# Performance work log

Hardware: AMD Instinct MI355X
Metric: run time of the kernel (lower is better)

## Reference

```python
import jax, jax.numpy as jnp
import numpy as np

B, S, E = 32, 128, 128
NQ, NS = 100000, 512
QN, SN = 4, 10
S_MAX = 4
NEG = -1e30


def setup_inputs() -> dict:
    key = jax.random.key(0)
    ks = jax.random.split(key, 24)
    def nrm(k, shape, sc):
        return jax.random.normal(k, shape, jnp.float32) * sc
    inp = {}
    inp['question'] = jax.random.randint(ks[0], (B, S), 0, NQ, jnp.int32)
    inp['response'] = jax.random.randint(ks[1], (B, S), 0, 2, jnp.int32)
    inp['mask'] = jax.random.randint(ks[2], (B, S), 0, 2, jnp.int32)
    inp['q_neighbors'] = jax.random.randint(ks[3], (NQ, QN), 0, NS, jnp.int32)
    inp['s_neighbors'] = jax.random.randint(ks[4], (NS, SN), 0, NQ, jnp.int32)
    sidx = jax.random.randint(ks[5], (NQ, S_MAX), 0, NS, jnp.int32)
    inp['qs_table'] = jnp.zeros((NQ, NS), jnp.float32).at[jnp.arange(NQ)[:, None], sidx].set(1.0)
    inp['emb_q'] = nrm(ks[6], (NQ, E), 1.0)
    inp['emb_s'] = nrm(ks[7], (NS, E), 1.0)
    inp['emb_r'] = nrm(ks[8], (2, E), 1.0)
    s_in = 1.0 / np.sqrt(2 * E).astype(np.float32)
    s_e = 1.0 / np.sqrt(E).astype(np.float32)
    inp['W_ih'] = nrm(ks[9], (4 * E, 2 * E), s_in)
    inp['b_ih'] = nrm(ks[10], (4 * E,), s_in)
    inp['b_hh'] = nrm(ks[11], (4 * E,), s_in)
    inp['W_agg'] = nrm(ks[12], (3, E, E), s_e)
    inp['b_agg'] = nrm(ks[13], (3, E), s_e)
    inp['W_last'] = nrm(ks[14], (E, E), s_e)
    inp['b_last'] = nrm(ks[15], (E,), s_e)
    inp['W_query'] = nrm(ks[16], (E, E), s_e)
    inp['b_query'] = nrm(ks[17], (E,), s_e)
    inp['W_key'] = nrm(ks[18], (E, E), s_e)
    inp['b_key'] = nrm(ks[19], (E,), s_e)
    inp['w_W'] = nrm(ks[20], (2 * E,), s_in)
    inp['b_W'] = nrm(ks[21], (), s_in)
    return inp


def _forward(question, response, mask, q_neighbors, s_neighbors, qs_table,
             emb_q, emb_s, emb_r, W_ih, b_ih, b_hh, W_agg, b_agg, W_last, b_last,
             W_query, b_query, W_key, b_key, w_W, b_W):
    Bq, Sq = question.shape
    Ed = emb_q.shape[1]
    AGG = W_agg.shape[0]
    w_q, w_k = w_W[:Ed], w_W[Ed:]
    c_pad = jnp.tanh(b_query) @ w_k  # attention logit piece of an all-zero padded state
    pos = jnp.arange(Sq)

    def step(state_history, xs):
        t, q_t, r_t, m_t, q_next = xs
        # ---- multi-hop neighbor gather (q -> s -> q -> s) ----
        n1 = q_neighbors[q_t]              # [B,QN] skill ids
        n2 = s_neighbors[n1]               # [B,QN,SN] question ids
        n3 = q_neighbors[n2]               # [B,QN,SN,QN] skill ids
        e = [emb_q[q_t], emb_s[n1], emb_q[n2], emb_s[n3]]
        # triangular mean-aggregate (dropout is identity in eval mode)
        for i in range(AGG):
            for j in range(AGG - i):
                e[j] = jnp.tanh((e[j + 1].mean(-2) + e[j]) @ W_agg[j].T + b_agg[j])
        agg = jnp.tanh(e[0] @ W_last.T + b_last)
        emb_qt = jnp.where((m_t == 1)[:, None], agg, emb_q[q_t])
        # ---- LSTMCell with zero initial (h, c): W_hh @ 0 drops out, b_hh remains ----
        x = jnp.concatenate([emb_qt, emb_r[r_t]], -1)
        gates = x @ W_ih.T + b_ih + b_hh
        gi, gf, gg, go = jnp.split(gates, 4, -1)
        h = jax.nn.sigmoid(go) * jnp.tanh(jax.nn.sigmoid(gi) * jnp.tanh(gg))
        # ---- skills related to next question; zero-padded rows contribute exactly 0 ----
        vals, sidx = jax.lax.top_k(qs_table[q_next], S_MAX)
        emb_sk = emb_s[sidx] * (vals > 0.0)[..., None]
        qs_concat = jnp.concatenate([emb_q[q_next][:, None], emb_sk], 1)  # [B,1+S_MAX,E]
        # ---- hard recap: history steps whose question is a 2-hop neighbor of q_next ----
        q_rel = s_neighbors[q_neighbors[q_next]].reshape(Bq, -1)          # [B,QN*SN]
        matches = (question[:, :, None] == q_rel[:, None, :]).any(-1) & (pos[None, :] < t)
        n_sel = matches.sum(-1)
        P = (jnp.max(n_sel) - n_sel).astype(jnp.float32)  # zero-pad count to per-batch max
        # ---- predict: MLP_W(concat(Q,K)) is rank-1 => logit = a[b,q] + c[b,s] ----
        a = jnp.tanh(qs_concat @ W_key.T + b_key) @ w_q + b_W             # [B,Qd]
        c_hist = jnp.tanh(state_history @ W_query.T + b_query) @ w_k      # [B,S]
        c_cur = jnp.tanh(h @ W_query.T + b_query) @ w_k                   # [B]
        lh = jnp.where(matches[:, None, :], a[:, :, None] + c_hist[:, None, :], NEG)
        lc = a + c_cur[:, None]
        lp = a + c_pad
        m = jnp.maximum(jnp.maximum(lh.max(-1), lc), lp)
        Eh = jnp.exp(lh - m[:, :, None])
        Ec = jnp.exp(lc - m)
        Ep = jnp.exp(lp - m)
        g_hist = jnp.einsum('bqe,bse->bqs', qs_concat, state_history)
        g_cur = jnp.einsum('bqe,be->bq', qs_concat, h)
        denom = Eh.sum(-1) + Ec + P[:, None] * Ep  # zero-pad states counted analytically
        num = (Eh * g_hist).sum(-1) + Ec * g_cur   # pads multiply g=0 -> no numerator term
        y = jax.nn.sigmoid(jnp.sum(num / denom, axis=1))
        # original skips the state write at t == 0 (slot 0 stays zero forever)
        state_history = state_history.at[:, t].set(jnp.where(t > 0, h, jnp.zeros_like(h)))
        return state_history, y

    ts = jnp.arange(Sq - 1)
    xs = (ts, question[:, :-1].T, response[:, :-1].T, mask[:, :-1].T, question[:, 1:].T)
    init = jnp.zeros((Bq, Sq, Ed), jnp.float32)
    _, ys = jax.lax.scan(step, init, xs)
    return jnp.zeros((Bq, Sq), jnp.float32).at[:, 0].set(0.5).at[:, 1:].set(ys.T)


def reference(question, response, mask, q_neighbors, s_neighbors, qs_table,
              emb_q, emb_s, emb_r, W_ih, b_ih, b_hh, W_agg, b_agg, W_last, b_last,
              W_query, b_query, W_key, b_key, w_W, b_W):
    return _forward(question, response, mask, q_neighbors, s_neighbors, qs_table,
                    emb_q, emb_s, emb_r, W_ih, b_ih, b_hh, W_agg, b_agg, W_last, b_last,
                    W_query, b_query, W_key, b_key, w_W, b_W)
```

## Files before the change

kernel.cpp:

```cpp
#include <hip/hip_runtime.h>
#include <stdint.h>

#define NB 32
#define SEQ 128
#define EMB 128
#define NSTEP 127
#define NS 512

__device__ __forceinline__ float ftanh(float x){ float e=__expf(2.f*x); return 1.f-2.f/(e+1.f); }
__device__ __forceinline__ float fsig(float x){ return 1.f/(1.f+__expf(-x)); }
__device__ __forceinline__ float4 ld4(const float* p){ return *(const float4*)p; }

#define FMA_COL(acc, xv) \
  acc.x = fmaf(xv.x, w0.x, fmaf(xv.y, w1.x, fmaf(xv.z, w2.x, fmaf(xv.w, w3.x, acc.x)))); \
  acc.y = fmaf(xv.x, w0.y, fmaf(xv.y, w1.y, fmaf(xv.z, w2.y, fmaf(xv.w, w3.y, acc.y)))); \
  acc.z = fmaf(xv.x, w0.z, fmaf(xv.y, w1.z, fmaf(xv.z, w2.z, fmaf(xv.w, w3.z, acc.z)))); \
  acc.w = fmaf(xv.x, w0.w, fmaf(xv.y, w1.w, fmaf(xv.z, w2.w, fmaf(xv.w, w3.w, acc.w))));

template<int K, int XS>
__device__ __forceinline__ void gemm8(const float* __restrict__ WT, int NEtot,
                                      const float* __restrict__ Xl,
                                      const float* __restrict__ bias,
                                      float* __restrict__ outb )
{
  const int tid = threadIdx.x;
  const int et = tid & 31;
  const int rt = tid >> 5;
  const float* wp = WT + et*4;
  const float* xr = Xl + rt*XS;
  constexpr int G = K/4;
  float4 acc = {0.f,0.f,0.f,0.f};
  float4 w0 = ld4(wp);
  float4 w1 = ld4(wp + NEtot);
  float4 w2 = ld4(wp + 2*NEtot);
  float4 w3 = ld4(wp + 3*NEtot);
  float4 xa = ld4(xr);
  #pragma unroll 4
  for (int g = 0; g < G-1; ++g) {
    const float* wn = wp + (size_t)(4*(g+1))*NEtot;
    float4 m0 = ld4(wn);
    float4 m1 = ld4(wn + NEtot);
    float4 m2 = ld4(wn + 2*NEtot);
    float4 m3 = ld4(wn + 3*NEtot);
    float4 xb = ld4(xr + 4*(g+1));
    FMA_COL(acc, xa);
    w0=m0; w1=m1; w2=m2; w3=m3; xa=xb;
  }
  FMA_COL(acc, xa);
  float4 bb = ld4(bias + et*4);
  acc.x+=bb.x; acc.y+=bb.y; acc.z+=bb.z; acc.w+=bb.w;
  *(float4*)(outb + rt*132 + et*4) = acc;
}
#undef FMA_COL

__global__ __launch_bounds__(256) void k_T(
    const float* __restrict__ W_agg, const float* __restrict__ W_last,
    const float* __restrict__ W_query, const float* __restrict__ W_ih,
    const float* __restrict__ b_ih, const float* __restrict__ b_hh,
    const float* __restrict__ b_query, const float* __restrict__ w_W,
    float* __restrict__ WT012, float* __restrict__ WLT, float* __restrict__ WQT,
    float* __restrict__ WIHT, float* __restrict__ BIH, float* __restrict__ CPAD,
    float* __restrict__ G1, int* __restrict__ Pmaxi)
{
  const int gid = blockIdx.x*256 + threadIdx.x;
  const int gsz = gridDim.x*256;
  for (int i = gid; i < 49152; i += gsz) {
    int j = i >> 14, rem = i & 16383, k = rem >> 7, e = rem & 127;
    WT012[i] = W_agg[j*16384 + e*128 + k];
  }
  for (int i = gid; i < 16384; i += gsz) {
    int k = i >> 7, e = i & 127;
    WLT[i] = W_last[e*128 + k];
    WQT[i] = W_query[e*128 + k];
  }
  for (int i = gid; i < 131072; i += gsz) {
    int k = i >> 9, e = i & 511;
    WIHT[i] = W_ih[e*256 + k];
  }
  for (int i = gid; i < 65536; i += gsz) G1[i] = 0.f;
  for (int i = gid; i < 512; i += gsz) BIH[i] = b_ih[i] + b_hh[i];
  for (int i = gid; i < 128; i += gsz) Pmaxi[i] = 0;
  if (blockIdx.x == 0) {
    __shared__ float red[256];
    float v = (threadIdx.x < 128) ? ftanh(b_query[threadIdx.x]) * w_W[128 + threadIdx.x] : 0.f;
    red[threadIdx.x] = v; __syncthreads();
    #pragma unroll
    for (int s = 128; s > 0; s >>= 1) {
      if (threadIdx.x < s) red[threadIdx.x] += red[threadIdx.x + s];
      __syncthreads();
    }
    if (threadIdx.x == 0) CPAD[0] = red[0];
  }
}

__global__ __launch_bounds__(256) void k_pre(
    const int* __restrict__ s_neighbors, const int* __restrict__ q_neighbors,
    const float* __restrict__ emb_q, const float* __restrict__ emb_s,
    const float* __restrict__ WT012, const float* __restrict__ b_agg,
    float* __restrict__ E1, float* __restrict__ G1)
{
  __shared__ float XA[8*132];
  __shared__ float XB[8*132];
  __shared__ int idx[80];
  __shared__ int n3[32];
  const int tid = threadIdx.x;
  const int blk = blockIdx.x;
  if (blk < 64) {
    const int s0 = blk*8;
    if (tid < 80) idx[tid] = s_neighbors[s0*10 + tid];
    __syncthreads();
    {
      int r = tid >> 5, e4 = (tid & 31) << 2;
      float4 a = ld4(emb_s + (size_t)(s0+r)*128 + e4);
      float sx=0,sy=0,sz=0,sw=0;
      #pragma unroll
      for (int jj = 0; jj < 10; ++jj) {
        float4 q = ld4(emb_q + (size_t)idx[r*10+jj]*128 + e4);
        sx+=q.x; sy+=q.y; sz+=q.z; sw+=q.w;
      }
      float4 o; o.x=a.x+0.1f*sx; o.y=a.y+0.1f*sy; o.z=a.z+0.1f*sz; o.w=a.w+0.1f*sw;
      *(float4*)(XA + r*132 + e4) = o;
    }
    __syncthreads();
    gemm8<128,132>(WT012 + 16384, 128, XA, b_agg + 128, XB);
    __syncthreads();
    for (int f = tid; f < 1024; f += 256) {
      int r = f >> 7, e = f & 127;
      E1[(size_t)(s0+r)*128 + e] = ftanh(XB[r*132 + e]);
    }
  } else {
    const int p0 = (blk-64)*8;
    if (tid < 8) idx[tid] = s_neighbors[p0 + tid];
    __syncthreads();
    if (tid < 32) n3[tid] = q_neighbors[(size_t)idx[tid>>2]*4 + (tid&3)];
    __syncthreads();
    {
      int r = tid >> 5, e4 = (tid & 31) << 2;
      float4 a = ld4(emb_q + (size_t)idx[r]*128 + e4);
      float sx=0,sy=0,sz=0,sw=0;
      #pragma unroll
      for (int k = 0; k < 4; ++k) {
        float4 q = ld4(emb_s + (size_t)n3[r*4+k]*128 + e4);
        sx+=q.x; sy+=q.y; sz+=q.z; sw+=q.w;
      }
      float4 o; o.x=a.x+0.25f*sx; o.y=a.y+0.25f*sy; o.z=a.z+0.25f*sz; o.w=a.w+0.25f*sw;
      *(float4*)(XA + r*132 + e4) = o;
    }
    __syncthreads();
    gemm8<128,132>(WT012 + 32768, 128, XA, b_agg + 256, XB);
    __syncthreads();
    for (int f = tid; f < 1024; f += 256) {
      int r = f >> 7, e = f & 127;
      atomicAdd(&G1[(size_t)((p0+r)/10)*128 + e], ftanh(XB[r*132 + e]));
    }
  }
}

__global__ __launch_bounds__(256) void k_pre2(
    const float* __restrict__ E1, const float* __restrict__ G1,
    const float* __restrict__ WT012, const float* __restrict__ b_agg,
    float* __restrict__ E2)
{
  __shared__ float XA[8*132];
  __shared__ float XB[8*132];
  const int tid = threadIdx.x;
  const int s0 = blockIdx.x*8;
  for (int f = tid; f < 1024; f += 256) {
    int r = f >> 7, e = f & 127;
    XA[r*132 + e] = 0.1f*G1[(size_t)(s0+r)*128 + e] + E1[(size_t)(s0+r)*128 + e];
  }
  __syncthreads();
  gemm8<128,132>(WT012 + 16384, 128, XA, b_agg + 128, XB);
  __syncthreads();
  for (int f = tid; f < 1024; f += 256) {
    int r = f >> 7, e = f & 127;
    E2[(size_t)(s0+r)*128 + e] = ftanh(XB[r*132 + e]);
  }
}

__global__ __launch_bounds__(256) void k_chain(
    const int* __restrict__ question, const int* __restrict__ response,
    const int* __restrict__ maskp, const int* __restrict__ q_neighbors,
    const float* __restrict__ emb_q, const float* __restrict__ emb_s,
    const float* __restrict__ emb_r,
    const float* __restrict__ WT012, const float* __restrict__ WLT,
    const float* __restrict__ WQT, const float* __restrict__ WIHT,
    const float* __restrict__ BIH,
    const float* __restrict__ b_agg, const float* __restrict__ b_last,
    const float* __restrict__ b_query, const float* __restrict__ w_W,
    const float* __restrict__ E1, const float* __restrict__ E2,
    float* __restrict__ Hfull, float* __restrict__ Cq)
{
  __shared__ float XA[8*132];
  __shared__ float XB[8*132];
  __shared__ float M1[8*132];
  __shared__ float M2[8*132];
  __shared__ float XC[8*264];
  __shared__ int qts[8], rts[8], mts[8], n1s[32];

  const int tid = threadIdx.x;
  const int blk = blockIdx.x;

  if (tid < 8) {
    int rid = blk*8 + tid;
    int b = rid / 127, t = rid - b*127;
    qts[tid] = question[b*SEQ + t];
    rts[tid] = response[b*SEQ + t];
    mts[tid] = maskp[b*SEQ + t];
  }
  __syncthreads();
  if (tid < 32) n1s[tid] = q_neighbors[(size_t)qts[tid>>2]*4 + (tid&3)];
  __syncthreads();
  {
    int r = tid >> 5, e4 = (tid & 31) << 2;
    const int* nn = n1s + r*4;
    float4 a = ld4(emb_q + (size_t)qts[r]*128 + e4);
    float s1x=0,s1y=0,s1z=0,s1w=0, s2x=0,s2y=0,s2z=0,s2w=0, s3x=0,s3y=0,s3z=0,s3w=0;
    #pragma unroll
    for (int i = 0; i < 4; ++i) {
      float4 q1 = ld4(emb_s + (size_t)nn[i]*128 + e4);
      float4 q2 = ld4(E1 + (size_t)nn[i]*128 + e4);
      float4 q3 = ld4(E2 + (size_t)nn[i]*128 + e4);
      s1x+=q1.x; s1y+=q1.y; s1z+=q1.z; s1w+=q1.w;
      s2x+=q2.x; s2y+=q2.y; s2z+=q2.z; s2w+=q2.w;
      s3x+=q3.x; s3y+=q3.y; s3z+=q3.z; s3w+=q3.w;
    }
    float4 o; o.x=a.x+0.25f*s1x; o.y=a.y+0.25f*s1y; o.z=a.z+0.25f*s1z; o.w=a.w+0.25f*s1w;
    *(float4*)(XA + r*132 + e4) = o;
    float4 p; p.x=0.25f*s2x; p.y=0.25f*s2y; p.z=0.25f*s2z; p.w=0.25f*s2w;
    *(float4*)(M1 + r*132 + e4) = p;
    float4 u; u.x=0.25f*s3x; u.y=0.25f*s3y; u.z=0.25f*s3z; u.w=0.25f*s3w;
    *(float4*)(M2 + r*132 + e4) = u;
  }
  __syncthreads();
  gemm8<128,132>(WT012, 128, XA, b_agg, XB);
  __syncthreads();
  for (int f = tid; f < 1056; f += 256) XB[f] = M1[f] + ftanh(XB[f]);
  __syncthreads();
  gemm8<128,132>(WT012, 128, XB, b_agg, XA);
  __syncthreads();
  for (int f = tid; f < 1056; f += 256) XA[f] = M2[f] + ftanh(XA[f]);
  __syncthreads();
  gemm8<128,132>(WT012, 128, XA, b_agg, XB);
  __syncthreads();
  for (int f = tid; f < 1056; f += 256) XB[f] = ftanh(XB[f]);
  __syncthreads();
  gemm8<128,132>(WLT, 128, XB, b_last, XA);
  __syncthreads();
  for (int f = tid; f < 1024; f += 256) {
    int r = f >> 7, e = f & 127;
    float agg = ftanh(XA[r*132 + e]);
    XC[r*264 + e] = (mts[r] == 1) ? agg : emb_q[(size_t)qts[r]*128 + e];
    XC[r*264 + 128 + e] = emb_r[rts[r]*128 + e];
  }
  __syncthreads();
  gemm8<256,264>(WIHT,       512, XC, BIH,       XA);
  gemm8<256,264>(WIHT + 256, 512, XC, BIH + 256, XB);
  gemm8<256,264>(WIHT + 384, 512, XC, BIH + 384, M1);
  __syncthreads();
  for (int f = tid; f < 1024; f += 256) {
    int r = f >> 7, e = f & 127;
    float gi = XA[r*132 + e], gg = XB[r*132 + e], go = M1[r*132 + e];
    float h = fsig(go) * ftanh(fsig(gi) * ftanh(gg));
    XC[r*264 + e] = h;
    Hfull[(size_t)(blk*8 + r)*128 + e] = h;
  }
  __syncthreads();
  gemm8<128,264>(WQT, 128, XC, b_query, XA);
  __syncthreads();
  {
    const int et = tid & 31, rt = tid >> 5;
    float4 o = ld4(XA + rt*132 + et*4);
    float4 wv = ld4(w_W + 128 + et*4);
    float s = ftanh(o.x)*wv.x + ftanh(o.y)*wv.y + ftanh(o.z)*wv.z + ftanh(o.w)*wv.w;
    #pragma unroll
    for (int off = 16; off > 0; off >>= 1) s += __shfl_down(s, off);
    if (et == 0) Cq[blk*8 + rt] = s;
  }
}

__global__ __launch_bounds__(128) void k_match(
    const int* __restrict__ question, const int* __restrict__ q_neighbors,
    const int* __restrict__ s_neighbors,
    int* __restrict__ nsel, unsigned long long* __restrict__ mwords,
    int* __restrict__ Pmaxi)
{
  __shared__ int nq[4];
  __shared__ int qr[40];
  __shared__ unsigned long long wv[2];
  const int tid = threadIdx.x;
  const int t = blockIdx.x;
  for (int bb = 0; bb < 8; ++bb) {
    const int b = blockIdx.y*8 + bb;
    const int q_next = question[b*SEQ + t + 1];
    if (tid < 4) nq[tid] = q_neighbors[(size_t)q_next*4 + tid];
    __syncthreads();
    if (tid < 40) qr[tid] = s_neighbors[(size_t)nq[tid/10]*10 + tid%10];
    __syncthreads();
    bool pred = false;
    if (tid < t) {
      int qp = question[b*SEQ + tid];
      #pragma unroll 8
      for (int i = 0; i < 40; ++i) pred |= (qp == qr[i]);
    }
    unsigned long long bal = __ballot(pred);
    if ((tid & 63) == 0) wv[tid >> 6] = bal;
    __syncthreads();
    if (tid == 0) {
      mwords[((size_t)b*NSTEP + t)*2 + 0] = wv[0];
      mwords[((size_t)b*NSTEP + t)*2 + 1] = wv[1];
      int ns = __popcll(wv[0]) + __popcll(wv[1]);
      nsel[b*NSTEP + t] = ns;
      atomicMax(&Pmaxi[t], ns);
    }
    __syncthreads();
  }
}

__device__ __forceinline__ float wredsum(float v) {
  #pragma unroll
  for (int o = 32; o > 0; o >>= 1) v += __shfl_down(v, o);
  return v;
}
__device__ __forceinline__ float wredmax(float v) {
  #pragma unroll
  for (int o = 32; o > 0; o >>= 1) v = fmaxf(v, __shfl_down(v, o));
  return v;
}

__global__ __launch_bounds__(128) void k_attn(
    const int* __restrict__ question, const float* __restrict__ qs_table,
    const float* __restrict__ emb_q, const float* __restrict__ emb_s,
    const float* __restrict__ CPAD,
    const float* __restrict__ Hfull, const float* __restrict__ Cq,
    const int* __restrict__ nsel, const unsigned long long* __restrict__ mwords,
    const int* __restrict__ Pmaxi, float* __restrict__ out)
{
  __shared__ float us[128];
  __shared__ int cols[8];
  __shared__ int cnt;
  __shared__ float smx[2];
  __shared__ float s3[2][3];
  const int tid = threadIdx.x;
  const int wid = tid >> 6;
  const int bid = blockIdx.x;
  const int b = bid / NSTEP, t = bid % NSTEP;
  const size_t bt = (size_t)b*NSTEP + t;
  const int q_next = question[b*SEQ + t + 1];

  if (tid == 0) cnt = 0;
  __syncthreads();
  #pragma unroll
  for (int m = 0; m < 4; ++m) {
    int c = tid + 128*m;
    float v = qs_table[(size_t)q_next*NS + c];
    if (v > 0.f) {
      int p = atomicAdd(&cnt, 1);
      if (p < 8) cols[p] = c;
    }
  }
  __syncthreads();
  const int nc = min(cnt, 4);
  {
    float ue = emb_q[(size_t)q_next*EMB + tid];
    for (int i = 0; i < nc; ++i) ue += emb_s[(size_t)cols[i]*EMB + tid];
    us[tid] = ue;
  }
  const float c_pad = CPAD[0];
  const float P = (float)(Pmaxi[t] - nsel[bt]);

  const unsigned long long w0 = mwords[bt*2 + 0];
  const unsigned long long w1 = mwords[bt*2 + 1];
  const bool matched = (tid < 64) ? ((w0 >> tid) & 1ull)
                                  : ((w1 >> (tid - 64)) & 1ull);
  const float c_cur = Cq[bt];
  float Cp = matched ? ((tid == 0) ? c_pad : Cq[(size_t)b*NSTEP + tid]) : -3.0e38f;
  float mh = wredmax(Cp);
  if ((tid & 63) == 0) smx[wid] = mh;
  __syncthreads();
  float M = fmaxf(fmaxf(smx[0], smx[1]), fmaxf(c_cur, c_pad));
  float wgt = matched ? __expf(Cp - M) : 0.f;
  float dotp = 0.f;
  if (matched && tid >= 1) {
    const float* hp = Hfull + ((size_t)b*NSTEP + tid)*EMB;
    float s = 0.f;
    #pragma unroll 8
    for (int e = 0; e < 128; e += 4) {
      float4 h4 = ld4(hp + e);
      s = fmaf(us[e],h4.x, fmaf(us[e+1],h4.y, fmaf(us[e+2],h4.z, fmaf(us[e+3],h4.w, s))));
    }
    dotp = s;
  }
  float gcp = us[tid] * Hfull[bt*EMB + tid];
  float a0 = wredsum(wgt);
  float a1 = wredsum(wgt * dotp);
  float a2 = wredsum(gcp);
  if ((tid & 63) == 0) { s3[wid][0] = a0; s3[wid][1] = a1; s3[wid][2] = a2; }
  __syncthreads();
  if (tid == 0) {
    float Sexp = s3[0][0] + s3[1][0];
    float Snum = s3[0][1] + s3[1][1];
    float gc   = s3[0][2] + s3[1][2];
    float Ec = __expf(c_cur - M), Ep = __expf(c_pad - M);
    float D = Sexp + Ec + P * Ep;
    float numt = Snum + Ec * gc;
    out[b*SEQ + t + 1] = fsig(numt / D);
    if (t == 0) out[b*SEQ] = 0.5f;
  }
}

extern "C" void kernel_launch(void* const* d_in, const int* in_sizes, int n_in,
                              void* d_out, int out_size, void* d_ws, size_t ws_size,
                              hipStream_t stream) {
  const int* question    = (const int*)d_in[0];
  const int* response    = (const int*)d_in[1];
  const int* maskp       = (const int*)d_in[2];
  const int* q_neighbors = (const int*)d_in[3];
  const int* s_neighbors = (const int*)d_in[4];
  const float* qs_table  = (const float*)d_in[5];
  const float* emb_q     = (const float*)d_in[6];
  const float* emb_s     = (const float*)d_in[7];
  const float* emb_r     = (const float*)d_in[8];
  const float* W_ih      = (const float*)d_in[9];
  const float* b_ih      = (const float*)d_in[10];
  const float* b_hh      = (const float*)d_in[11];
  const float* W_agg     = (const float*)d_in[12];
  const float* b_agg     = (const float*)d_in[13];
  const float* W_last    = (const float*)d_in[14];
  const float* b_last    = (const float*)d_in[15];
  const float* W_query   = (const float*)d_in[16];
  const float* b_query   = (const float*)d_in[17];
  const float* w_W       = (const float*)d_in[20];
  float* out = (float*)d_out;

  float* ws = (float*)d_ws;
  float* WT012 = ws;
  float* WLT   = ws + 49152;
  float* WQT   = ws + 65536;
  float* WIHT  = ws + 81920;
  float* BIH   = ws + 212992;
  float* CPAD  = ws + 213504;
  float* E1    = ws + 213520;
  float* G1    = ws + 279056;
  float* E2    = ws + 344592;
  float* Hfull = ws + 410128;
  float* Cq    = ws + 930320;
  int*   Pmaxi = (int*)(ws + 934384);
  int*   nselp = (int*)(ws + 934512);
  unsigned long long* mwords =
      (unsigned long long*)(((uintptr_t)(ws + 938576) + 15) & ~(uintptr_t)15);

  k_T<<<dim3(64), dim3(256), 0, stream>>>(
      W_agg, W_last, W_query, W_ih, b_ih, b_hh, b_query, w_W,
      WT012, WLT, WQT, WIHT, BIH, CPAD, G1, Pmaxi);
  k_pre<<<dim3(704), dim3(256), 0, stream>>>(
      s_neighbors, q_neighbors, emb_q, emb_s, WT012, b_agg, E1, G1);
  k_pre2<<<dim3(64), dim3(256), 0, stream>>>(E1, G1, WT012, b_agg, E2);
  k_chain<<<dim3(508), dim3(256), 0, stream>>>(
      question, response, maskp, q_neighbors, emb_q, emb_s, emb_r,
      WT012, WLT, WQT, WIHT, BIH, b_agg, b_last, b_query, w_W,
      E1, E2, Hfull, Cq);
  k_match<<<dim3(NSTEP, 4), dim3(128), 0, stream>>>(
      question, q_neighbors, s_neighbors, nselp, mwords, Pmaxi);
  k_attn<<<dim3(NB*NSTEP), dim3(128), 0, stream>>>(
      question, qs_table, emb_q, emb_s, CPAD, Hfull, Cq,
      nselp, mwords, Pmaxi, out);
}
```

Before: 433.8 us.

## Deepen gemm8 weight prefetch, parallelize k_match per batch, vectorize qs_table scan

The gemm8 inner loop now prefetches weights two K-groups ahead with two register sets, so more loads are in flight per FMA block. k_match launches one 64-thread wave per (step, batch) pair instead of looping over 8 batches with 128 threads, which removes the per-batch barriers and exposes more parallelism. k_attn reads its qs_table row with one float4 load per thread instead of four scalar loads. The deeper prefetch uses more registers, and k_match now launches many more small blocks.

```diff
diff --git a/kernel.cpp b/kernel.cpp
--- a/kernel.cpp
+++ b/kernel.cpp
@@ -11,11 +11,11 @@
 __device__ __forceinline__ float fsig(float x){ return 1.f/(1.f+__expf(-x)); }
 __device__ __forceinline__ float4 ld4(const float* p){ return *(const float4*)p; }
 
-#define FMA_COL(acc, xv) \
-  acc.x = fmaf(xv.x, w0.x, fmaf(xv.y, w1.x, fmaf(xv.z, w2.x, fmaf(xv.w, w3.x, acc.x)))); \
-  acc.y = fmaf(xv.x, w0.y, fmaf(xv.y, w1.y, fmaf(xv.z, w2.y, fmaf(xv.w, w3.y, acc.y)))); \
-  acc.z = fmaf(xv.x, w0.z, fmaf(xv.y, w1.z, fmaf(xv.z, w2.z, fmaf(xv.w, w3.z, acc.z)))); \
-  acc.w = fmaf(xv.x, w0.w, fmaf(xv.y, w1.w, fmaf(xv.z, w2.w, fmaf(xv.w, w3.w, acc.w))));
+#define FMA4(acc, xv, a0, a1, a2, a3) \
+  acc.x = fmaf(xv.x, a0.x, fmaf(xv.y, a1.x, fmaf(xv.z, a2.x, fmaf(xv.w, a3.x, acc.x)))); \
+  acc.y = fmaf(xv.x, a0.y, fmaf(xv.y, a1.y, fmaf(xv.z, a2.y, fmaf(xv.w, a3.y, acc.y)))); \
+  acc.z = fmaf(xv.x, a0.z, fmaf(xv.y, a1.z, fmaf(xv.z, a2.z, fmaf(xv.w, a3.z, acc.z)))); \
+  acc.w = fmaf(xv.x, a0.w, fmaf(xv.y, a1.w, fmaf(xv.z, a2.w, fmaf(xv.w, a3.w, acc.w))));
 
 template<int K, int XS>
 __device__ __forceinline__ void gemm8(const float* __restrict__ WT, int NEtot,
@@ -34,24 +34,40 @@
   float4 w1 = ld4(wp + NEtot);
   float4 w2 = ld4(wp + 2*NEtot);
   float4 w3 = ld4(wp + 3*NEtot);
-  float4 xa = ld4(xr);
-  #pragma unroll 4
-  for (int g = 0; g < G-1; ++g) {
-    const float* wn = wp + (size_t)(4*(g+1))*NEtot;
-    float4 m0 = ld4(wn);
-    float4 m1 = ld4(wn + NEtot);
-    float4 m2 = ld4(wn + 2*NEtot);
-    float4 m3 = ld4(wn + 3*NEtot);
+  const float* wq = wp + (size_t)4*NEtot;
+  float4 m0 = ld4(wq);
+  float4 m1 = ld4(wq + NEtot);
+  float4 m2 = ld4(wq + 2*NEtot);
+  float4 m3 = ld4(wq + 3*NEtot);
+  #pragma unroll 2
+  for (int g = 0; g + 2 < G; g += 2) {
+    const float* wa = wp + (size_t)(4*(g+2))*NEtot;
+    float4 n0 = ld4(wa);
+    float4 n1 = ld4(wa + NEtot);
+    float4 n2 = ld4(wa + 2*NEtot);
+    float4 n3 = ld4(wa + 3*NEtot);
+    float4 xa = ld4(xr + 4*g);
+    FMA4(acc, xa, w0, w1, w2, w3);
+    w0=n0; w1=n1; w2=n2; w3=n3;
+    const float* wb = wp + (size_t)(4*(g+3))*NEtot;
+    float4 o0 = ld4(wb);
+    float4 o1 = ld4(wb + NEtot);
+    float4 o2 = ld4(wb + 2*NEtot);
+    float4 o3 = ld4(wb + 3*NEtot);
     float4 xb = ld4(xr + 4*(g+1));
-    FMA_COL(acc, xa);
-    w0=m0; w1=m1; w2=m2; w3=m3; xa=xb;
-  }
-  FMA_COL(acc, xa);
+    FMA4(acc, xb, m0, m1, m2, m3);
+    m0=o0; m1=o1; m2=o2; m3=o3;
+  }
+  {
+    float4 xa = ld4(xr + 4*(G-2));
+    FMA4(acc, xa, w0, w1, w2, w3);
+    float4 xb = ld4(xr + 4*(G-1));
+    FMA4(acc, xb, m0, m1, m2, m3);
+  }
   float4 bb = ld4(bias + et*4);
   acc.x+=bb.x; acc.y+=bb.y; acc.z+=bb.z; acc.w+=bb.w;
   *(float4*)(outb + rt*132 + et*4) = acc;
 }
-#undef FMA_COL
 
 __global__ __launch_bounds__(256) void k_T(
     const float* __restrict__ W_agg, const float* __restrict__ W_last,
@@ -279,41 +295,35 @@
   }
 }
 
-__global__ __launch_bounds__(128) void k_match(
+__global__ __launch_bounds__(64) void k_match(
     const int* __restrict__ question, const int* __restrict__ q_neighbors,
     const int* __restrict__ s_neighbors,
     int* __restrict__ nsel, unsigned long long* __restrict__ mwords,
     int* __restrict__ Pmaxi)
 {
-  __shared__ int nq[4];
   __shared__ int qr[40];
-  __shared__ unsigned long long wv[2];
   const int tid = threadIdx.x;
   const int t = blockIdx.x;
-  for (int bb = 0; bb < 8; ++bb) {
-    const int b = blockIdx.y*8 + bb;
-    const int q_next = question[b*SEQ + t + 1];
-    if (tid < 4) nq[tid] = q_neighbors[(size_t)q_next*4 + tid];
-    __syncthreads();
-    if (tid < 40) qr[tid] = s_neighbors[(size_t)nq[tid/10]*10 + tid%10];
-    __syncthreads();
-    bool pred = false;
-    if (tid < t) {
-      int qp = question[b*SEQ + tid];
-      #pragma unroll 8
-      for (int i = 0; i < 40; ++i) pred |= (qp == qr[i]);
-    }
-    unsigned long long bal = __ballot(pred);
-    if ((tid & 63) == 0) wv[tid >> 6] = bal;
-    __syncthreads();
-    if (tid == 0) {
-      mwords[((size_t)b*NSTEP + t)*2 + 0] = wv[0];
-      mwords[((size_t)b*NSTEP + t)*2 + 1] = wv[1];
-      int ns = __popcll(wv[0]) + __popcll(wv[1]);
-      nsel[b*NSTEP + t] = ns;
-      atomicMax(&Pmaxi[t], ns);
-    }
-    __syncthreads();
+  const int b = blockIdx.y;
+  const int q_next = question[b*SEQ + t + 1];
+  if (tid < 40)
+    qr[tid] = s_neighbors[(size_t)q_neighbors[(size_t)q_next*4 + tid/10]*10 + tid%10];
+  __syncthreads();
+  int q0 = question[b*SEQ + tid];
+  int q1 = question[b*SEQ + 64 + tid];
+  bool p0 = false, p1 = false;
+  #pragma unroll 8
+  for (int i = 0; i < 40; ++i) { p0 |= (q0 == qr[i]); p1 |= (q1 == qr[i]); }
+  p0 &= (tid < t);
+  p1 &= (64 + tid < t);
+  unsigned long long w0 = __ballot(p0);
+  unsigned long long w1 = __ballot(p1);
+  if (tid == 0) {
+    mwords[((size_t)b*NSTEP + t)*2 + 0] = w0;
+    mwords[((size_t)b*NSTEP + t)*2 + 1] = w1;
+    int ns = __popcll(w0) + __popcll(w1);
+    nsel[b*NSTEP + t] = ns;
+    atomicMax(&Pmaxi[t], ns);
   }
 }
 
@@ -350,14 +360,12 @@
 
   if (tid == 0) cnt = 0;
   __syncthreads();
-  #pragma unroll
-  for (int m = 0; m < 4; ++m) {
-    int c = tid + 128*m;
-    float v = qs_table[(size_t)q_next*NS + c];
-    if (v > 0.f) {
-      int p = atomicAdd(&cnt, 1);
-      if (p < 8) cols[p] = c;
-    }
+  {
+    float4 v = ld4(qs_table + (size_t)q_next*NS + tid*4);
+    if (v.x > 0.f) { int p = atomicAdd(&cnt, 1); if (p < 8) cols[p] = tid*4; }
+    if (v.y > 0.f) { int p = atomicAdd(&cnt, 1); if (p < 8) cols[p] = tid*4+1; }
+    if (v.z > 0.f) { int p = atomicAdd(&cnt, 1); if (p < 8) cols[p] = tid*4+2; }
+    if (v.w > 0.f) { int p = atomicAdd(&cnt, 1); if (p < 8) cols[p] = tid*4+3; }
   }
   __syncthreads();
   const int nc = min(cnt, 4);
@@ -460,7 +468,7 @@
       question, response, maskp, q_neighbors, emb_q, emb_s, emb_r,
       WT012, WLT, WQT, WIHT, BIH, b_agg, b_last, b_query, w_W,
       E1, E2, Hfull, Cq);
-  k_match<<<dim3(NSTEP, 4), dim3(128), 0, stream>>>(
+  k_match<<<dim3(NSTEP, NB), dim3(64), 0, stream>>>(
       question, q_neighbors, s_neighbors, nselp, mwords, Pmaxi);
   k_attn<<<dim3(NB*NSTEP), dim3(128), 0, stream>>>(
       question, qs_table, emb_q, emb_s, CPAD, Hfull, Cq,
```

New measurement: 430.1 us. Within noise of the previous version (-0.8%).
